# Optimization experiments

Hardware: AMD Instinct MI355X
Metric: run time of the kernel (lower is better)

The kernel has to match this reference:

```python
import jax, jax.numpy as jnp
import numpy as np

N = 50000; E = 800000; F_IN = 512; H = 2; C1 = 128; C2 = 32; N_CLASS = 32; N_HID = 64
LOSS_WEIGHT = 0.5


def _layer_norm(x, g, b):
    m = x.mean(-1, keepdims=True)
    v = ((x - m) ** 2).mean(-1, keepdims=True)
    return (x - m) / jnp.sqrt(v + 1e-5) * g + b


def _gat_conv(x, src, dst, n, W, Wh1, bh1, Wh2, bh2, heads, c, concat):
    # x: [n, in]; src/dst: [E'] (self loops already appended)
    xt = (x @ W).reshape(n, heads, c)            # [n, H, C]
    xj = xt[src]                                  # [E', H, C] gathered source feats
    # scaled dot-product attention logits per edge/head
    e = jnp.einsum('ehc,ehc->eh', xt[dst], xj) / np.float32(np.sqrt(c))
    m = jax.ops.segment_max(e, dst, num_segments=n)
    ex = jnp.exp(e - m[dst])
    s = jax.ops.segment_sum(ex, dst, num_segments=n)
    alpha = ex / (s[dst] + 1e-16)                 # [E', H]
    out = jax.ops.segment_sum(alpha[:, :, None] * xj, dst, num_segments=n)  # [n, H, C]
    # per-head auxiliary class prediction head h (DeepGAT)
    h = jax.nn.elu(jnp.einsum('nhc,cd->nhd', xt, Wh1) + bh1)
    h = jnp.einsum('nhd,dk->nhk', h, Wh2) + bh2   # [n, H, n_class]
    out = out.reshape(n, heads * c) if concat else out.mean(axis=1)
    return out, h, alpha


def setup_inputs() -> dict:
    key = jax.random.key(0)
    ks = jax.random.split(key, 24)
    g = lambda k, shape, fan: jax.random.normal(k, shape, jnp.float32) / np.float32(np.sqrt(fan))
    d = {}
    d['x'] = jax.random.normal(ks[0], (N, F_IN), jnp.float32)
    d['edge_index'] = jax.random.randint(ks[1], (2, E), 0, N, jnp.int32)
    # layer 1: F_IN -> H*C1 (concat)
    d['W1'] = g(ks[2], (F_IN, H * C1), F_IN)
    d['Wh1a'] = g(ks[3], (C1, N_HID), C1); d['bh1a'] = jnp.zeros((N_HID,), jnp.float32)
    d['Wh2a'] = g(ks[4], (N_HID, N_CLASS), N_HID); d['bh2a'] = jnp.zeros((N_CLASS,), jnp.float32)
    d['g1'] = jnp.ones((H * C1,), jnp.float32); d['b1'] = jnp.zeros((H * C1,), jnp.float32)
    # layer 2: H*C1 -> H*C2 (concat)
    d['W2'] = g(ks[5], (H * C1, H * C2), H * C1)
    d['Wh1b'] = g(ks[6], (C2, N_HID), C2); d['bh1b'] = jnp.zeros((N_HID,), jnp.float32)
    d['Wh2b'] = g(ks[7], (N_HID, N_CLASS), N_HID); d['bh2b'] = jnp.zeros((N_CLASS,), jnp.float32)
    d['g2'] = jnp.ones((H * C2,), jnp.float32); d['b2'] = jnp.zeros((H * C2,), jnp.float32)
    # layer 3: H*C2 -> N_CLASS (mean over heads)
    d['W3'] = g(ks[8], (H * C2, H * N_CLASS), H * C2)
    d['Wh1c'] = g(ks[9], (N_CLASS, N_HID), N_CLASS); d['bh1c'] = jnp.zeros((N_HID,), jnp.float32)
    d['Wh2c'] = g(ks[10], (N_HID, N_CLASS), N_HID); d['bh2c'] = jnp.zeros((N_CLASS,), jnp.float32)
    d['g3'] = jnp.ones((N_CLASS,), jnp.float32); d['b3'] = jnp.zeros((N_CLASS,), jnp.float32)
    return d


def reference(x, edge_index, W1, Wh1a, bh1a, Wh2a, bh2a, g1, b1,
              W2, Wh1b, bh1b, Wh2b, bh2b, g2, b2,
              W3, Wh1c, bh1c, Wh2c, bh2c, g3, b3):
    n = x.shape[0]
    loops = jnp.arange(n, dtype=edge_index.dtype)
    src = jnp.concatenate([edge_index[0], loops])
    dst = jnp.concatenate([edge_index[1], loops])
    # eval mode: F.dropout is identity
    x1, h1, _ = _gat_conv(x, src, dst, n, W1, Wh1a, bh1a, Wh2a, bh2a, H, C1, True)
    x1 = jax.nn.elu(_layer_norm(x1, g1, b1))
    x2, h2, _ = _gat_conv(x1, src, dst, n, W2, Wh1b, bh1b, Wh2b, bh2b, H, C2, True)
    x2 = jax.nn.elu(_layer_norm(x2, g2, b2))
    x3, h3, alpha = _gat_conv(x2, src, dst, n, W3, Wh1c, bh1c, Wh2c, bh2c, H, N_CLASS, False)
    x3 = _layer_norm(x3, g3, b3)
    return (x3, h1, h2 * LOSS_WEIGHT, h3, alpha)
```

## Files before the change

kernel.cpp:

```cpp
#include <hip/hip_runtime.h>

#define NN 50000
#define EE 800000
#define EPN 850000

typedef __attribute__((ext_vector_type(8))) short bf16x8;
typedef __attribute__((ext_vector_type(4))) float f32x4;
typedef unsigned short ushort_t;

__device__ __forceinline__ float eluf(float v) { return v > 0.f ? v : expm1f(v); }
__device__ __forceinline__ unsigned short f2bf(float f) {
  unsigned u = __float_as_uint(f);
  unsigned r = (u + 0x7FFFu + ((u >> 16) & 1u)) >> 16;
  return (unsigned short)r;
}
__device__ __forceinline__ float bf2f(unsigned short b) {
  return __uint_as_float(((unsigned)b) << 16);
}
__device__ __forceinline__ void unpack8(uint4 u, float* o) {
  o[0] = __uint_as_float(u.x << 16); o[1] = __uint_as_float(u.x & 0xFFFF0000u);
  o[2] = __uint_as_float(u.y << 16); o[3] = __uint_as_float(u.y & 0xFFFF0000u);
  o[4] = __uint_as_float(u.z << 16); o[5] = __uint_as_float(u.z & 0xFFFF0000u);
  o[6] = __uint_as_float(u.w << 16); o[7] = __uint_as_float(u.w & 0xFFFF0000u);
}
__device__ __forceinline__ void gload_lds16(const ushort_t* g, ushort_t* l) {
  __builtin_amdgcn_global_load_lds((const __attribute__((address_space(1))) void*)g,
                                   (__attribute__((address_space(3))) void*)l, 16, 0, 0);
}

__global__ __launch_bounds__(256) void conv_w1(const float* __restrict__ W,
                                               ushort_t* __restrict__ Wc) {
  int idx = blockIdx.x * 256 + threadIdx.x;
  if (idx >= 256 * 1024) return;
  int col = idx >> 10, rem = idx & 1023;
  int kb = rem >> 6, j = rem & 63;
  int sel = j >> 5, k = j & 31;
  int gk = kb * 32 + k;
  float v = W[(size_t)gk * 256 + col];
  unsigned short h = f2bf(v);
  Wc[idx] = sel ? (ushort_t)f2bf(v - bf2f(h)) : h;
}

__global__ __launch_bounds__(512) void gemm1_mfma(const float* __restrict__ A,
                                                  const ushort_t* __restrict__ Wc,
                                                  ushort_t* __restrict__ C16, int M) {
  constexpr int K = 512;
  __shared__ alignas(16) ushort_t Bs[2][128 * 64];
  int tid = threadIdx.x;
  int w = tid >> 6, lane = tid & 63, l15 = lane & 15, l4 = lane >> 4;
  int row0 = blockIdx.y * 128, col0 = blockIdx.x * 128;
  int arow = row0 + w * 16 + l15;
  int arowc = arow < M ? arow : M - 1;
  const float* arp = A + (size_t)arowc * K + l4 * 8;

  int chunk_src = (lane & 7) ^ ((lane >> 3) & 7);
  const ushort_t* wsrc =
      Wc + (size_t)(col0 + w * 16 + (lane >> 3)) * 1024 + chunk_src * 8;
  ushort_t* ldst0 = &Bs[0][(w * 16) * 64];
  ushort_t* ldst1 = &Bs[1][(w * 16) * 64];

  int swz = l15 & 7;
  int roff_h = ((l4 ^ swz) << 3);
  int roff_l = (((l4 | 4) ^ swz) << 3);
  int rbase = l15 * 64;

  f32x4 acc[8];
#pragma unroll
  for (int t = 0; t < 8; ++t) acc[t] = (f32x4){0.f, 0.f, 0.f, 0.f};

#pragma unroll
  for (int q = 0; q < 2; ++q) gload_lds16(wsrc + q * 8192, ldst0 + q * 512);
  float4 pa0c = *(const float4*)(arp);
  float4 pa1c = *(const float4*)(arp + 4);
  float4 pa0n, pa1n;

  for (int k0 = 0; k0 < K; k0 += 32) {
    int kb = k0 >> 5, p = kb & 1;
    __syncthreads();
    if (k0 + 32 < K) {
      ushort_t* dst = (p ? ldst0 : ldst1);
      const ushort_t* src = wsrc + (kb + 1) * 64;
#pragma unroll
      for (int q = 0; q < 2; ++q) gload_lds16(src + q * 8192, dst + q * 512);
      pa0n = *(const float4*)(arp + k0 + 32);
      pa1n = *(const float4*)(arp + k0 + 36);
    }
    bf16x8 ah, al;
    {
      float v[8] = {pa0c.x, pa0c.y, pa0c.z, pa0c.w, pa1c.x, pa1c.y, pa1c.z, pa1c.w};
#pragma unroll
      for (int i = 0; i < 8; ++i) {
        unsigned short h = f2bf(v[i]);
        ah[i] = (short)h;
        al[i] = (short)f2bf(v[i] - bf2f(h));
      }
    }
    const ushort_t* bp = &Bs[p][rbase];
#pragma unroll
    for (int t = 0; t < 8; ++t) {
      bf16x8 b_h = *(const bf16x8*)&bp[t * 1024 + roff_h];
      bf16x8 b_l = *(const bf16x8*)&bp[t * 1024 + roff_l];
      acc[t] = __builtin_amdgcn_mfma_f32_16x16x32_bf16(ah, b_h, acc[t], 0, 0, 0);
      acc[t] = __builtin_amdgcn_mfma_f32_16x16x32_bf16(ah, b_l, acc[t], 0, 0, 0);
      acc[t] = __builtin_amdgcn_mfma_f32_16x16x32_bf16(al, b_h, acc[t], 0, 0, 0);
    }
    pa0c = pa0n; pa1c = pa1n;
  }
#pragma unroll
  for (int t = 0; t < 8; ++t) {
#pragma unroll
    for (int r = 0; r < 4; ++r) {
      int grow = row0 + w * 16 + l4 * 4 + r;
      if (grow < M) C16[(size_t)grow * 256 + col0 + t * 16 + l15] = f2bf(acc[t][r]);
    }
  }
}

template <int NT>
__global__ __launch_bounds__(256) void gemm_mfma(const float* __restrict__ A,
                                                 const float* __restrict__ B,
                                                 ushort_t* __restrict__ C16,
                                                 int M, int N, int K) {
  __shared__ unsigned short Ah[64 * 40], Al[64 * 40];
  __shared__ unsigned short Bh[NT * 16 * 40], Bl[NT * 16 * 40];
  int tid = threadIdx.x;
  int wave = tid >> 6, lane = tid & 63;
  int l15 = lane & 15, l4 = lane >> 4;
  int row0 = blockIdx.y * 64, col0 = blockIdx.x * (NT * 16);

  f32x4 acc[NT];
#pragma unroll
  for (int t = 0; t < NT; ++t) acc[t] = (f32x4){0.f, 0.f, 0.f, 0.f};

  int ar = tid >> 2;
  int ak = (tid & 3) * 8;
  constexpr int TPC = 256 / (NT * 16);
  constexpr int NK = 32 / TPC;
  int bc = tid / TPC;
  int bk = (tid % TPC) * NK;

  for (int k0 = 0; k0 < K; k0 += 32) {
    {
      float v[8];
      int grow = row0 + ar;
      if (grow < M) {
        float4 q0 = *(const float4*)&A[(size_t)grow * K + k0 + ak];
        float4 q1 = *(const float4*)&A[(size_t)grow * K + k0 + ak + 4];
        v[0] = q0.x; v[1] = q0.y; v[2] = q0.z; v[3] = q0.w;
        v[4] = q1.x; v[5] = q1.y; v[6] = q1.z; v[7] = q1.w;
      } else {
#pragma unroll
        for (int i = 0; i < 8; ++i) v[i] = 0.f;
      }
      bf16x8 hv, lv;
#pragma unroll
      for (int i = 0; i < 8; ++i) {
        unsigned short h = f2bf(v[i]);
        hv[i] = (short)h;
        lv[i] = (short)f2bf(v[i] - bf2f(h));
      }
      *(bf16x8*)&Ah[ar * 40 + ak] = hv;
      *(bf16x8*)&Al[ar * 40 + ak] = lv;
    }
    {
#pragma unroll
      for (int i = 0; i < NK; ++i) {
        float v = B[(size_t)(k0 + bk + i) * N + col0 + bc];
        unsigned short h = f2bf(v);
        Bh[bc * 40 + bk + i] = h;
        Bl[bc * 40 + bk + i] = f2bf(v - bf2f(h));
      }
    }
    __syncthreads();
    bf16x8 a_h = *(const bf16x8*)&Ah[(wave * 16 + l15) * 40 + l4 * 8];
    bf16x8 a_l = *(const bf16x8*)&Al[(wave * 16 + l15) * 40 + l4 * 8];
#pragma unroll
    for (int t = 0; t < NT; ++t) {
      bf16x8 b_h = *(const bf16x8*)&Bh[(t * 16 + l15) * 40 + l4 * 8];
      bf16x8 b_l = *(const bf16x8*)&Bl[(t * 16 + l15) * 40 + l4 * 8];
      acc[t] = __builtin_amdgcn_mfma_f32_16x16x32_bf16(a_h, b_h, acc[t], 0, 0, 0);
      acc[t] = __builtin_amdgcn_mfma_f32_16x16x32_bf16(a_h, b_l, acc[t], 0, 0, 0);
      acc[t] = __builtin_amdgcn_mfma_f32_16x16x32_bf16(a_l, b_h, acc[t], 0, 0, 0);
    }
    __syncthreads();
  }
#pragma unroll
  for (int t = 0; t < NT; ++t) {
#pragma unroll
    for (int r = 0; r < 4; ++r) {
      int grow = row0 + wave * 16 + l4 * 4 + r;
      if (grow < M) C16[(size_t)grow * N + col0 + t * 16 + l15] = f2bf(acc[t][r]);
    }
  }
}

template <int C>
__global__ __launch_bounds__(256) void aux_mfma(const ushort_t* __restrict__ xt16,
                                                const float* __restrict__ Wh1,
                                                const float* __restrict__ bh1,
                                                const float* __restrict__ Wh2,
                                                const float* __restrict__ bh2,
                                                float* __restrict__ hout,
                                                float scale) {
  constexpr int KS = C / 32;
  constexpr int LDB = C + 8;
  constexpr int UNION_B = 64 * LDB * 2 * 2;
  constexpr int UNION_H = 64 * 72 * 2 * 2;
  constexpr int UNION = UNION_B > UNION_H ? UNION_B : UNION_H;
  __shared__ alignas(16) char smem[9216 + UNION];
  ushort_t* w2h = (ushort_t*)smem;
  ushort_t* w2l = w2h + 32 * 72;
  ushort_t* BhS = (ushort_t*)(smem + 9216);
  ushort_t* BlS = BhS + 64 * LDB;
  ushort_t* hidh = (ushort_t*)(smem + 9216);
  ushort_t* hidl = hidh + 64 * 72;

  int tid = threadIdx.x;
  for (int i = tid; i < C * 64; i += 256) {
    int k = i >> 6, col = i & 63;
    float v = Wh1[i];
    unsigned short h = f2bf(v);
    BhS[col * LDB + k] = h;
    BlS[col * LDB + k] = f2bf(v - bf2f(h));
  }
  for (int i = tid; i < 64 * 32; i += 256) {
    int k = i >> 5, col = i & 31;
    float v = Wh2[i];
    unsigned short h = f2bf(v);
    w2h[col * 72 + k] = h;
    w2l[col * 72 + k] = f2bf(v - bf2f(h));
  }
  __syncthreads();

  int w = tid >> 6, lane = tid & 63, l15 = lane & 15, l4 = lane >> 4;
  int gr = blockIdx.x * 64 + w * 16 + l15;
  const int M2 = 2 * NN;

  f32x4 acc[4];
#pragma unroll
  for (int t = 0; t < 4; ++t) acc[t] = (f32x4){0.f, 0.f, 0.f, 0.f};

#pragma unroll
  for (int ks = 0; ks < KS; ++ks) {
    bf16x8 ah;
    if (gr < M2) {
      ah = *(const bf16x8*)(xt16 + (size_t)gr * C + ks * 32 + l4 * 8);
    } else {
      ah = (bf16x8){0, 0, 0, 0, 0, 0, 0, 0};
    }
#pragma unroll
    for (int t = 0; t < 4; ++t) {
      bf16x8 b_h = *(const bf16x8*)&BhS[(t * 16 + l15) * LDB + ks * 32 + l4 * 8];
      bf16x8 b_l = *(const bf16x8*)&BlS[(t * 16 + l15) * LDB + ks * 32 + l4 * 8];
      acc[t] = __builtin_amdgcn_mfma_f32_16x16x32_bf16(ah, b_h, acc[t], 0, 0, 0);
      acc[t] = __builtin_amdgcn_mfma_f32_16x16x32_bf16(ah, b_l, acc[t], 0, 0, 0);
    }
  }
  __syncthreads();
#pragma unroll
  for (int t = 0; t < 4; ++t) {
    float bb = bh1[t * 16 + l15];
#pragma unroll
    for (int r = 0; r < 4; ++r) {
      float h = eluf(acc[t][r] + bb);
      unsigned short hh = f2bf(h);
      int row = w * 16 + l4 * 4 + r, col = t * 16 + l15;
      hidh[row * 72 + col] = hh;
      hidl[row * 72 + col] = f2bf(h - bf2f(hh));
    }
  }
  __syncthreads();
  f32x4 acc2[2];
  acc2[0] = (f32x4){0.f, 0.f, 0.f, 0.f};
  acc2[1] = acc2[0];
#pragma unroll
  for (int ks = 0; ks < 2; ++ks) {
    bf16x8 ah = *(const bf16x8*)&hidh[(w * 16 + l15) * 72 + ks * 32 + l4 * 8];
    bf16x8 al = *(const bf16x8*)&hidl[(w * 16 + l15) * 72 + ks * 32 + l4 * 8];
#pragma unroll
    for (int t2 = 0; t2 < 2; ++t2) {
      bf16x8 b_h = *(const bf16x8*)&w2h[(t2 * 16 + l15) * 72 + ks * 32 + l4 * 8];
      bf16x8 b_l = *(const bf16x8*)&w2l[(t2 * 16 + l15) * 72 + ks * 32 + l4 * 8];
      acc2[t2] = __builtin_amdgcn_mfma_f32_16x16x32_bf16(ah, b_h, acc2[t2], 0, 0, 0);
      acc2[t2] = __builtin_amdgcn_mfma_f32_16x16x32_bf16(ah, b_l, acc2[t2], 0, 0, 0);
      acc2[t2] = __builtin_amdgcn_mfma_f32_16x16x32_bf16(al, b_h, acc2[t2], 0, 0, 0);
    }
  }
#pragma unroll
  for (int t2 = 0; t2 < 2; ++t2) {
    int col = t2 * 16 + l15;
    float bb = bh2[col];
#pragma unroll
    for (int r = 0; r < 4; ++r) {
      int gr2 = blockIdx.x * 64 + w * 16 + l4 * 4 + r;
      if (gr2 < M2)
        hout[(size_t)(gr2 >> 1) * 64 + (gr2 & 1) * 32 + col] = (acc2[t2][r] + bb) * scale;
    }
  }
}

__global__ __launch_bounds__(256) void hist_kernel(const int* __restrict__ ei,
                                                   int* __restrict__ cnt) {
  int e = blockIdx.x * 256 + threadIdx.x;
  if (e >= EPN) return;
  int d = (e < EE) ? ei[EE + e] : e - EE;
  atomicAdd(&cnt[d], 1);
}

__global__ __launch_bounds__(1024) void scan_blocks(const int* __restrict__ cnt,
                                                    int* __restrict__ tmp,
                                                    int* __restrict__ bsum) {
  __shared__ int lds[1024];
  int t = threadIdx.x, idx = blockIdx.x * 1024 + t;
  int v = (idx < NN) ? cnt[idx] : 0;
  lds[t] = v;
  __syncthreads();
  for (int off = 1; off < 1024; off <<= 1) {
    int add = (t >= off) ? lds[t - off] : 0;
    __syncthreads();
    lds[t] += add;
    __syncthreads();
  }
  if (idx < NN) tmp[idx] = lds[t];
  if (t == 1023) bsum[blockIdx.x] = lds[t];
}

__global__ __launch_bounds__(64) void scan_bsum(int* __restrict__ bsum, int nb) {
  int t = threadIdx.x;
  int v = (t < nb) ? bsum[t] : 0;
#pragma unroll
  for (int off = 1; off < 64; off <<= 1) {
    int u = __shfl_up(v, off);
    if (t >= off) v += u;
  }
  if (t < nb) bsum[t] = v;
}

__global__ __launch_bounds__(256) void scan_final(const int* __restrict__ cnt,
                                                  const int* __restrict__ tmp,
                                                  const int* __restrict__ bsum,
                                                  int* __restrict__ rowptr,
                                                  int* __restrict__ fill) {
  int idx = blockIdx.x * 256 + threadIdx.x;
  if (idx >= NN) return;
  int b = idx >> 10;
  int off = (b > 0) ? bsum[b - 1] : 0;
  int inc = tmp[idx] + off;
  rowptr[idx + 1] = inc;
  fill[idx] = inc - cnt[idx];
  if (idx == 0) rowptr[0] = 0;
}

__global__ __launch_bounds__(256) void scatter_kernel(const int* __restrict__ ei,
                                                      int* __restrict__ fill,
                                                      int* __restrict__ eids,
                                                      int* __restrict__ srcs) {
  int e = blockIdx.x * 256 + threadIdx.x;
  if (e >= EPN) return;
  int d, s;
  if (e < EE) { d = ei[EE + e]; s = ei[e]; } else { d = s = e - EE; }
  int pos = atomicAdd(&fill[d], 1);
  eids[pos] = e;
  srcs[pos] = s;
}

__global__ __launch_bounds__(256) void gat256_fused(const ushort_t* __restrict__ xt16,
                                                    const int* __restrict__ srcs,
                                                    const int* __restrict__ rowptr,
                                                    float* __restrict__ outb,
                                                    const float* __restrict__ g,
                                                    const float* __restrict__ b) {
  int node = (int)((blockIdx.x * (size_t)blockDim.x + threadIdx.x) >> 6);
  int lane = threadIdx.x & 63;
  if (node >= NN) return;
  int l32 = lane & 31, half = lane >> 5;
  int start = rowptr[node], end = rowptr[node + 1];
  float dv[8];
  unpack8(*(const uint4*)(xt16 + (size_t)node * 256 + l32 * 8), dv);
  float m = -3e38f, s_h = 0.f;
  float acc[8] = {0.f, 0.f, 0.f, 0.f, 0.f, 0.f, 0.f, 0.f};

  int i = start;
  for (; i + 8 <= end; i += 8) {
    int sj[4];
    float sv[4][8];
    float p[4];
#pragma unroll
    for (int q = 0; q < 4; ++q) sj[q] = srcs[i + q * 2 + half];
#pragma unroll
    for (int q = 0; q < 4; ++q)
      unpack8(*(const uint4*)(xt16 + (size_t)sj[q] * 256 + l32 * 8), sv[q]);
#pragma unroll
    for (int q = 0; q < 4; ++q) {
      float p_ = 0.f;
#pragma unroll
      for (int k = 0; k < 8; ++k) p_ = fmaf(sv[q][k], dv[k], p_);
      p_ += __shfl_xor(p_, 1); p_ += __shfl_xor(p_, 2);
      p_ += __shfl_xor(p_, 4); p_ += __shfl_xor(p_, 8);
      p[q] = p_ * 0.08838834764831843f;
    }
    float pm = fmaxf(fmaxf(p[0], p[1]), fmaxf(p[2], p[3]));
    if (__any(pm > m + 8.f)) {
#pragma unroll
      for (int q = 0; q < 4; ++q) {
        float pb = fmaxf(p[q], __shfl_xor(p[q], 32));
        float mn = fmaxf(m, pb);
        float scf = __expf(m - mn), w = __expf(p[q] - mn);
        s_h = s_h * scf + w;
#pragma unroll
        for (int k = 0; k < 8; ++k) acc[k] = fmaf(w, sv[q][k], acc[k] * scf);
        m = mn;
      }
    } else {
#pragma unroll
      for (int q = 0; q < 4; ++q) {
        float w = __expf(p[q] - m);
        s_h += w;
#pragma unroll
        for (int k = 0; k < 8; ++k) acc[k] = fmaf(w, sv[q][k], acc[k]);
      }
    }
  }
  for (; i < end; i += 2) {
    bool valid = (i + half) < end;
    int sj = srcs[valid ? i + half : i];
    float sv[8];
    unpack8(*(const uint4*)(xt16 + (size_t)sj * 256 + l32 * 8), sv);
    float p_ = 0.f;
#pragma unroll
    for (int k = 0; k < 8; ++k) p_ = fmaf(sv[k], dv[k], p_);
    p_ += __shfl_xor(p_, 1); p_ += __shfl_xor(p_, 2);
    p_ += __shfl_xor(p_, 4); p_ += __shfl_xor(p_, 8);
    p_ *= 0.08838834764831843f;
    if (!valid) p_ = -3e38f;
    float pb = fmaxf(p_, __shfl_xor(p_, 32));
    float mn = fmaxf(m, pb);
    float scf = __expf(m - mn);
    float w = valid ? __expf(p_ - mn) : 0.f;
    s_h = s_h * scf + w;
#pragma unroll
    for (int k = 0; k < 8; ++k) acc[k] = fmaf(w, sv[k], acc[k] * scf);
    m = mn;
  }
  float s = s_h + __shfl_xor(s_h, 32);
#pragma unroll
  for (int k = 0; k < 8; ++k) acc[k] += __shfl_xor(acc[k], 32);
  float inv = 1.f / (s + 1e-16f);
  float v[8];
#pragma unroll
  for (int k = 0; k < 8; ++k) v[k] = acc[k] * inv;
  float sum = 0.f;
#pragma unroll
  for (int k = 0; k < 8; ++k) sum += v[k];
  sum += __shfl_xor(sum, 1); sum += __shfl_xor(sum, 2); sum += __shfl_xor(sum, 4);
  sum += __shfl_xor(sum, 8); sum += __shfl_xor(sum, 16);
  float mean = sum * (1.f / 256.f);
  float q = 0.f;
#pragma unroll
  for (int k = 0; k < 8; ++k) { v[k] -= mean; q = fmaf(v[k], v[k], q); }
  q += __shfl_xor(q, 1); q += __shfl_xor(q, 2); q += __shfl_xor(q, 4);
  q += __shfl_xor(q, 8); q += __shfl_xor(q, 16);
  float rstd = rsqrtf(q * (1.f / 256.f) + 1e-5f);
  if (half == 0) {
    float4 ga = *(const float4*)&g[l32 * 8], gb = *(const float4*)&g[l32 * 8 + 4];
    float4 ba = *(const float4*)&b[l32 * 8], bb = *(const float4*)&b[l32 * 8 + 4];
    float4 r0, r1;
    r0.x = eluf(v[0] * rstd * ga.x + ba.x); r0.y = eluf(v[1] * rstd * ga.y + ba.y);
    r0.z = eluf(v[2] * rstd * ga.z + ba.z); r0.w = eluf(v[3] * rstd * ga.w + ba.w);
    r1.x = eluf(v[4] * rstd * gb.x + bb.x); r1.y = eluf(v[5] * rstd * gb.y + bb.y);
    r1.z = eluf(v[6] * rstd * gb.z + bb.z); r1.w = eluf(v[7] * rstd * gb.w + bb.w);
    *(float4*)(outb + (size_t)node * 256 + l32 * 8) = r0;
    *(float4*)(outb + (size_t)node * 256 + l32 * 8 + 4) = r1;
  }
}

template <int MODE>
__global__ __launch_bounds__(256) void gat64_t(const ushort_t* __restrict__ xt16,
                                               const int* __restrict__ srcs,
                                               const int* __restrict__ eids,
                                               const int* __restrict__ rowptr,
                                               float* __restrict__ outf,
                                               float* __restrict__ logit_out,
                                               float* __restrict__ mbuf,
                                               float* __restrict__ sbuf,
                                               const float* __restrict__ g,
                                               const float* __restrict__ b) {
  __shared__ alignas(16) float wbuf[4][64];
  int wv = threadIdx.x >> 6;
  int node = (int)((blockIdx.x * (size_t)blockDim.x + threadIdx.x) >> 6);
  int lane = threadIdx.x & 63;
  if (node >= NN) return;
  int l32 = lane & 31, half = lane >> 5;
  int start = rowptr[node], end = rowptr[node + 1];
  float dv[32];
  {
    const ushort_t* dp = xt16 + (size_t)node * 64 + half * 32;
    unpack8(*(const uint4*)(dp), dv);
    unpack8(*(const uint4*)(dp + 8), dv + 8);
    unpack8(*(const uint4*)(dp + 16), dv + 16);
    unpack8(*(const uint4*)(dp + 24), dv + 24);
  }
  float m = -3e38f, s = 0.f, acc = 0.f;

  for (int base = start; base < end; base += 32) {
    int cnt = end - base;
    cnt = cnt > 32 ? 32 : cnt;
    int sidx = srcs[base + (l32 < cnt ? l32 : 0)];
    float sv[32];
    {
      const ushort_t* sp = xt16 + (size_t)sidx * 64 + half * 32;
      unpack8(*(const uint4*)(sp), sv);
      unpack8(*(const uint4*)(sp + 8), sv + 8);
      unpack8(*(const uint4*)(sp + 16), sv + 16);
      unpack8(*(const uint4*)(sp + 24), sv + 24);
    }
    float p = 0.f;
#pragma unroll
    for (int k = 0; k < 32; ++k) p = fmaf(sv[k], dv[k], p);
    p *= 0.17677669529663687f;
    if (MODE == 1) {
      if (l32 < cnt) logit_out[(size_t)eids[base + l32] * 2 + half] = p;
    }
    if (l32 >= cnt) p = -3e38f;
    float bm = p;
    bm = fmaxf(bm, __shfl_xor(bm, 1));
    bm = fmaxf(bm, __shfl_xor(bm, 2));
    bm = fmaxf(bm, __shfl_xor(bm, 4));
    bm = fmaxf(bm, __shfl_xor(bm, 8));
    bm = fmaxf(bm, __shfl_xor(bm, 16));
    float mn = fmaxf(m, bm);
    float scf = __expf(m - mn);
    float w = (l32 < cnt) ? __expf(p - mn) : 0.f;
    wbuf[wv][(half << 5) + l32] = w;
    float bs = w;
    bs += __shfl_xor(bs, 1);
    bs += __shfl_xor(bs, 2);
    bs += __shfl_xor(bs, 4);
    bs += __shfl_xor(bs, 8);
    bs += __shfl_xor(bs, 16);
    s = s * scf + bs;
    acc *= scf;
    m = mn;
    int nb4 = cnt & ~3;
    const float* wp = &wbuf[wv][(half << 5)];
    for (int e = 0; e < nb4; e += 4) {
      float4 w4 = *(const float4*)(wp + e);
      int s0 = srcs[base + e + 0];
      int s1 = srcs[base + e + 1];
      int s2 = srcs[base + e + 2];
      int s3 = srcs[base + e + 3];
      acc = fmaf(w4.x, bf2f(xt16[(size_t)s0 * 64 + lane]), acc);
      acc = fmaf(w4.y, bf2f(xt16[(size_t)s1 * 64 + lane]), acc);
      acc = fmaf(w4.z, bf2f(xt16[(size_t)s2 * 64 + lane]), acc);
      acc = fmaf(w4.w, bf2f(xt16[(size_t)s3 * 64 + lane]), acc);
    }
    for (int e = nb4; e < cnt; ++e) {
      float wq = wp[e];
      int sj = srcs[base + e];
      acc = fmaf(wq, bf2f(xt16[(size_t)sj * 64 + lane]), acc);
    }
  }
  float inv = 1.f / (s + 1e-16f);
  float v = acc * inv;
  if (MODE == 0) {
    float sum = v;
#pragma unroll
    for (int o = 1; o < 64; o <<= 1) sum += __shfl_xor(sum, o);
    float mean = sum * (1.f / 64.f);
    float dvv = v - mean;
    float q = dvv * dvv;
#pragma unroll
    for (int o = 1; o < 64; o <<= 1) q += __shfl_xor(q, o);
    float rstd = rsqrtf(q * (1.f / 64.f) + 1e-5f);
    outf[(size_t)node * 64 + lane] = eluf(dvv * rstd * g[lane] + b[lane]);
  } else {
    if (l32 == 0) {
      mbuf[(size_t)node * 2 + half] = m;
      sbuf[(size_t)node * 2 + half] = s;
    }
    float t = __shfl_xor(v, 32);
    float y = 0.5f * (v + t);
    float sum = y;
#pragma unroll
    for (int o = 1; o < 32; o <<= 1) sum += __shfl_xor(sum, o);
    float mean = sum * (1.f / 32.f);
    float dy = y - mean;
    float q = dy * dy;
#pragma unroll
    for (int o = 1; o < 32; o <<= 1) q += __shfl_xor(q, o);
    float rstd = rsqrtf(q * (1.f / 32.f) + 1e-5f);
    if (half == 0) outf[(size_t)node * 32 + l32] = dy * rstd * g[l32] + b[l32];
  }
}

__global__ __launch_bounds__(256) void alpha_fix(float* __restrict__ al,
                                                 const int* __restrict__ ei,
                                                 const float* __restrict__ mbuf,
                                                 const float* __restrict__ sbuf) {
  size_t i = blockIdx.x * (size_t)blockDim.x + threadIdx.x;
  if (i >= (size_t)EPN * 2) return;
  int e = (int)(i >> 1), h = (int)(i & 1);
  int d = (e < EE) ? ei[EE + e] : e - EE;
  al[i] = expf(al[i] - mbuf[(size_t)d * 2 + h]) / (sbuf[(size_t)d * 2 + h] + 1e-16f);
}

extern "C" void kernel_launch(void* const* d_in, const int* in_sizes, int n_in,
                              void* d_out, int out_size, void* d_ws, size_t ws_size,
                              hipStream_t stream) {
  const float* x    = (const float*)d_in[0];
  const int*   ei   = (const int*)d_in[1];
  const float* W1   = (const float*)d_in[2];
  const float* Wh1a = (const float*)d_in[3];
  const float* bh1a = (const float*)d_in[4];
  const float* Wh2a = (const float*)d_in[5];
  const float* bh2a = (const float*)d_in[6];
  const float* g1   = (const float*)d_in[7];
  const float* b1   = (const float*)d_in[8];
  const float* W2   = (const float*)d_in[9];
  const float* Wh1b = (const float*)d_in[10];
  const float* bh1b = (const float*)d_in[11];
  const float* Wh2b = (const float*)d_in[12];
  const float* bh2b = (const float*)d_in[13];
  const float* g2   = (const float*)d_in[14];
  const float* b2   = (const float*)d_in[15];
  const float* W3   = (const float*)d_in[16];
  const float* Wh1c = (const float*)d_in[17];
  const float* bh1c = (const float*)d_in[18];
  const float* Wh2c = (const float*)d_in[19];
  const float* bh2c = (const float*)d_in[20];
  const float* g3   = (const float*)d_in[21];
  const float* b3   = (const float*)d_in[22];

  float* out  = (float*)d_out;
  float* o_x3 = out;
  float* o_h1 = out + (size_t)NN * 32;
  float* o_h2 = o_h1 + (size_t)NN * 64;
  float* o_h3 = o_h2 + (size_t)NN * 64;
  float* o_al = o_h3 + (size_t)NN * 64;

  float* ws  = (float*)d_ws;
  float* A   = ws;
  float* Bb  = ws + (size_t)NN * 256;
  int* cnt    = (int*)(Bb + (size_t)NN * 256);
  int* rowptr = cnt + NN;
  int* fill   = rowptr + NN + 1;
  int* eids   = fill + NN;
  int* srcs   = eids + EPN;
  int* tmp    = srcs + EPN;
  int* bsum   = tmp + NN;
  float* mbuf = (float*)(bsum + 64);
  float* sbuf = mbuf + (size_t)NN * 2;
  ushort_t* W1c = (ushort_t*)(sbuf + (size_t)NN * 2);
  ushort_t* A16 = (ushort_t*)A;

  dim3 blk(256);
  int gEdges = (EPN + 255) / 256;
  int gNodeW = (NN * 64 + 255) / 256;
  int gRows = (NN + 63) / 64;
  int gRows128 = (NN + 127) / 128;
  int gPairs = (int)(((size_t)EPN * 2 + 255) / 256);
  int gAux = (2 * NN + 63) / 64;
  int nbScan = (NN + 1023) / 1024;

  conv_w1<<<1024, blk, 0, stream>>>(W1, W1c);
  hipMemsetAsync(cnt, 0, (size_t)NN * 4, stream);
  hist_kernel<<<gEdges, blk, 0, stream>>>(ei, cnt);
  scan_blocks<<<nbScan, 1024, 0, stream>>>(cnt, tmp, bsum);
  scan_bsum<<<1, 64, 0, stream>>>(bsum, nbScan);
  scan_final<<<(NN + 255) / 256, blk, 0, stream>>>(cnt, tmp, bsum, rowptr, fill);
  scatter_kernel<<<gEdges, blk, 0, stream>>>(ei, fill, eids, srcs);

  gemm1_mfma<<<dim3(2, gRows128), 512, 0, stream>>>(x, W1c, A16, NN);
  aux_mfma<128><<<gAux, blk, 0, stream>>>(A16, Wh1a, bh1a, Wh2a, bh2a, o_h1, 1.0f);
  gat256_fused<<<gNodeW, blk, 0, stream>>>(A16, srcs, rowptr, Bb, g1, b1);

  gemm_mfma<4><<<dim3(1, gRows), blk, 0, stream>>>(Bb, W2, A16, NN, 64, 256);
  aux_mfma<32><<<gAux, blk, 0, stream>>>(A16, Wh1b, bh1b, Wh2b, bh2b, o_h2, 0.5f);
  gat64_t<0><<<gNodeW, blk, 0, stream>>>(A16, srcs, nullptr, rowptr, Bb, nullptr,
                                         nullptr, nullptr, g2, b2);

  gemm_mfma<4><<<dim3(1, gRows), blk, 0, stream>>>(Bb, W3, A16, NN, 64, 64);
  aux_mfma<32><<<gAux, blk, 0, stream>>>(A16, Wh1c, bh1c, Wh2c, bh2c, o_h3, 1.0f);
  gat64_t<1><<<gNodeW, blk, 0, stream>>>(A16, srcs, eids, rowptr, o_x3, o_al,
                                         mbuf, sbuf, g3, b3);
  alpha_fix<<<gPairs, blk, 0, stream>>>(o_al, ei, mbuf, sbuf);
}
```

Measured before the change: 478.1 us.

## Horizontally fuse aux prediction head and GAT aggregation kernels per layer

Merges the per-layer auxiliary MLP head kernel and the GAT aggregation kernel into one launch. Blocks are interleaved so that one aux block runs alongside every eight aggregation blocks, and both reuse a shared static LDS buffer. The aim is to remove three kernel launches and let the compute-bound MFMA head overlap the memory-bound gather. The cost is that every aggregation block now reserves about 45 KB of LDS, which limits how many blocks fit on a CU for the latency-sensitive gather work.

```diff
diff --git a/kernel.cpp b/kernel.cpp
--- a/kernel.cpp
+++ b/kernel.cpp
@@ -195,19 +195,15 @@
 }
 
 template <int C>
-__global__ __launch_bounds__(256) void aux_mfma(const ushort_t* __restrict__ xt16,
-                                                const float* __restrict__ Wh1,
-                                                const float* __restrict__ bh1,
-                                                const float* __restrict__ Wh2,
-                                                const float* __restrict__ bh2,
-                                                float* __restrict__ hout,
-                                                float scale) {
+__device__ __forceinline__ void aux_body(char* smem, int bid,
+                                         const ushort_t* __restrict__ xt16,
+                                         const float* __restrict__ Wh1,
+                                         const float* __restrict__ bh1,
+                                         const float* __restrict__ Wh2,
+                                         const float* __restrict__ bh2,
+                                         float* __restrict__ hout, float scale) {
   constexpr int KS = C / 32;
   constexpr int LDB = C + 8;
-  constexpr int UNION_B = 64 * LDB * 2 * 2;
-  constexpr int UNION_H = 64 * 72 * 2 * 2;
-  constexpr int UNION = UNION_B > UNION_H ? UNION_B : UNION_H;
-  __shared__ alignas(16) char smem[9216 + UNION];
   ushort_t* w2h = (ushort_t*)smem;
   ushort_t* w2l = w2h + 32 * 72;
   ushort_t* BhS = (ushort_t*)(smem + 9216);
@@ -233,7 +229,7 @@
   __syncthreads();
 
   int w = tid >> 6, lane = tid & 63, l15 = lane & 15, l4 = lane >> 4;
-  int gr = blockIdx.x * 64 + w * 16 + l15;
+  int gr = bid * 64 + w * 16 + l15;
   const int M2 = 2 * NN;
 
   f32x4 acc[4];
@@ -292,85 +288,20 @@
     float bb = bh2[col];
 #pragma unroll
     for (int r = 0; r < 4; ++r) {
-      int gr2 = blockIdx.x * 64 + w * 16 + l4 * 4 + r;
+      int gr2 = bid * 64 + w * 16 + l4 * 4 + r;
       if (gr2 < M2)
         hout[(size_t)(gr2 >> 1) * 64 + (gr2 & 1) * 32 + col] = (acc2[t2][r] + bb) * scale;
     }
   }
 }
 
-__global__ __launch_bounds__(256) void hist_kernel(const int* __restrict__ ei,
-                                                   int* __restrict__ cnt) {
-  int e = blockIdx.x * 256 + threadIdx.x;
-  if (e >= EPN) return;
-  int d = (e < EE) ? ei[EE + e] : e - EE;
-  atomicAdd(&cnt[d], 1);
-}
-
-__global__ __launch_bounds__(1024) void scan_blocks(const int* __restrict__ cnt,
-                                                    int* __restrict__ tmp,
-                                                    int* __restrict__ bsum) {
-  __shared__ int lds[1024];
-  int t = threadIdx.x, idx = blockIdx.x * 1024 + t;
-  int v = (idx < NN) ? cnt[idx] : 0;
-  lds[t] = v;
-  __syncthreads();
-  for (int off = 1; off < 1024; off <<= 1) {
-    int add = (t >= off) ? lds[t - off] : 0;
-    __syncthreads();
-    lds[t] += add;
-    __syncthreads();
-  }
-  if (idx < NN) tmp[idx] = lds[t];
-  if (t == 1023) bsum[blockIdx.x] = lds[t];
-}
-
-__global__ __launch_bounds__(64) void scan_bsum(int* __restrict__ bsum, int nb) {
-  int t = threadIdx.x;
-  int v = (t < nb) ? bsum[t] : 0;
-#pragma unroll
-  for (int off = 1; off < 64; off <<= 1) {
-    int u = __shfl_up(v, off);
-    if (t >= off) v += u;
-  }
-  if (t < nb) bsum[t] = v;
-}
-
-__global__ __launch_bounds__(256) void scan_final(const int* __restrict__ cnt,
-                                                  const int* __restrict__ tmp,
-                                                  const int* __restrict__ bsum,
-                                                  int* __restrict__ rowptr,
-                                                  int* __restrict__ fill) {
-  int idx = blockIdx.x * 256 + threadIdx.x;
-  if (idx >= NN) return;
-  int b = idx >> 10;
-  int off = (b > 0) ? bsum[b - 1] : 0;
-  int inc = tmp[idx] + off;
-  rowptr[idx + 1] = inc;
-  fill[idx] = inc - cnt[idx];
-  if (idx == 0) rowptr[0] = 0;
-}
-
-__global__ __launch_bounds__(256) void scatter_kernel(const int* __restrict__ ei,
-                                                      int* __restrict__ fill,
-                                                      int* __restrict__ eids,
-                                                      int* __restrict__ srcs) {
-  int e = blockIdx.x * 256 + threadIdx.x;
-  if (e >= EPN) return;
-  int d, s;
-  if (e < EE) { d = ei[EE + e]; s = ei[e]; } else { d = s = e - EE; }
-  int pos = atomicAdd(&fill[d], 1);
-  eids[pos] = e;
-  srcs[pos] = s;
-}
-
-__global__ __launch_bounds__(256) void gat256_fused(const ushort_t* __restrict__ xt16,
-                                                    const int* __restrict__ srcs,
-                                                    const int* __restrict__ rowptr,
-                                                    float* __restrict__ outb,
-                                                    const float* __restrict__ g,
-                                                    const float* __restrict__ b) {
-  int node = (int)((blockIdx.x * (size_t)blockDim.x + threadIdx.x) >> 6);
+__device__ __forceinline__ void gat256_body(int bid, const ushort_t* __restrict__ xt16,
+                                            const int* __restrict__ srcs,
+                                            const int* __restrict__ rowptr,
+                                            float* __restrict__ outb,
+                                            const float* __restrict__ g,
+                                            const float* __restrict__ b) {
+  int node = (int)(((size_t)bid * 256 + threadIdx.x) >> 6);
   int lane = threadIdx.x & 63;
   if (node >= NN) return;
   int l32 = lane & 31, half = lane >> 5;
@@ -475,19 +406,19 @@
 }
 
 template <int MODE>
-__global__ __launch_bounds__(256) void gat64_t(const ushort_t* __restrict__ xt16,
-                                               const int* __restrict__ srcs,
-                                               const int* __restrict__ eids,
-                                               const int* __restrict__ rowptr,
-                                               float* __restrict__ outf,
-                                               float* __restrict__ logit_out,
-                                               float* __restrict__ mbuf,
-                                               float* __restrict__ sbuf,
-                                               const float* __restrict__ g,
-                                               const float* __restrict__ b) {
-  __shared__ alignas(16) float wbuf[4][64];
+__device__ __forceinline__ void gat64_body(float (*wbuf)[64], int bid,
+                                           const ushort_t* __restrict__ xt16,
+                                           const int* __restrict__ srcs,
+                                           const int* __restrict__ eids,
+                                           const int* __restrict__ rowptr,
+                                           float* __restrict__ outf,
+                                           float* __restrict__ logit_out,
+                                           float* __restrict__ mbuf,
+                                           float* __restrict__ sbuf,
+                                           const float* __restrict__ g,
+                                           const float* __restrict__ b) {
   int wv = threadIdx.x >> 6;
-  int node = (int)((blockIdx.x * (size_t)blockDim.x + threadIdx.x) >> 6);
+  int node = (int)(((size_t)bid * 256 + threadIdx.x) >> 6);
   int lane = threadIdx.x & 63;
   if (node >= NN) return;
   int l32 = lane & 31, half = lane >> 5;
@@ -593,6 +524,123 @@
   }
 }
 
+#define A_AUX 1563
+#define G_GAT 12500
+
+__global__ __launch_bounds__(256) void fused_l1(const ushort_t* __restrict__ xt16,
+                                                const float* __restrict__ Wh1,
+                                                const float* __restrict__ bh1,
+                                                const float* __restrict__ Wh2,
+                                                const float* __restrict__ bh2,
+                                                float* __restrict__ hout,
+                                                const int* __restrict__ srcs,
+                                                const int* __restrict__ rowptr,
+                                                float* __restrict__ outb,
+                                                const float* __restrict__ g,
+                                                const float* __restrict__ b) {
+  __shared__ alignas(16) char smem[46080];
+  int k = blockIdx.x, grp = k / 9, pos = k - grp * 9;
+  if (pos == 0) {
+    aux_body<128>(smem, grp, xt16, Wh1, bh1, Wh2, bh2, hout, 1.0f);
+  } else {
+    int gid = grp * 8 + pos - 1;
+    if (gid < G_GAT) gat256_body(gid, xt16, srcs, rowptr, outb, g, b);
+  }
+}
+
+template <int MODE>
+__global__ __launch_bounds__(256) void fused_l23(const ushort_t* __restrict__ xt16,
+                                                 const float* __restrict__ Wh1,
+                                                 const float* __restrict__ bh1,
+                                                 const float* __restrict__ Wh2,
+                                                 const float* __restrict__ bh2,
+                                                 float* __restrict__ hout, float scale,
+                                                 const int* __restrict__ srcs,
+                                                 const int* __restrict__ eids,
+                                                 const int* __restrict__ rowptr,
+                                                 float* __restrict__ outf,
+                                                 float* __restrict__ logit_out,
+                                                 float* __restrict__ mbuf,
+                                                 float* __restrict__ sbuf,
+                                                 const float* __restrict__ g,
+                                                 const float* __restrict__ b) {
+  __shared__ alignas(16) char smem[46080];
+  int k = blockIdx.x, grp = k / 9, pos = k - grp * 9;
+  if (pos == 0) {
+    aux_body<32>(smem, grp, xt16, Wh1, bh1, Wh2, bh2, hout, scale);
+  } else {
+    int gid = grp * 8 + pos - 1;
+    if (gid < G_GAT)
+      gat64_body<MODE>((float(*)[64])smem, gid, xt16, srcs, eids, rowptr, outf,
+                       logit_out, mbuf, sbuf, g, b);
+  }
+}
+
+__global__ __launch_bounds__(256) void hist_kernel(const int* __restrict__ ei,
+                                                   int* __restrict__ cnt) {
+  int e = blockIdx.x * 256 + threadIdx.x;
+  if (e >= EPN) return;
+  int d = (e < EE) ? ei[EE + e] : e - EE;
+  atomicAdd(&cnt[d], 1);
+}
+
+__global__ __launch_bounds__(1024) void scan_blocks(const int* __restrict__ cnt,
+                                                    int* __restrict__ tmp,
+                                                    int* __restrict__ bsum) {
+  __shared__ int lds[1024];
+  int t = threadIdx.x, idx = blockIdx.x * 1024 + t;
+  int v = (idx < NN) ? cnt[idx] : 0;
+  lds[t] = v;
+  __syncthreads();
+  for (int off = 1; off < 1024; off <<= 1) {
+    int add = (t >= off) ? lds[t - off] : 0;
+    __syncthreads();
+    lds[t] += add;
+    __syncthreads();
+  }
+  if (idx < NN) tmp[idx] = lds[t];
+  if (t == 1023) bsum[blockIdx.x] = lds[t];
+}
+
+__global__ __launch_bounds__(64) void scan_bsum(int* __restrict__ bsum, int nb) {
+  int t = threadIdx.x;
+  int v = (t < nb) ? bsum[t] : 0;
+#pragma unroll
+  for (int off = 1; off < 64; off <<= 1) {
+    int u = __shfl_up(v, off);
+    if (t >= off) v += u;
+  }
+  if (t < nb) bsum[t] = v;
+}
+
+__global__ __launch_bounds__(256) void scan_final(const int* __restrict__ cnt,
+                                                  const int* __restrict__ tmp,
+                                                  const int* __restrict__ bsum,
+                                                  int* __restrict__ rowptr,
+                                                  int* __restrict__ fill) {
+  int idx = blockIdx.x * 256 + threadIdx.x;
+  if (idx >= NN) return;
+  int b = idx >> 10;
+  int off = (b > 0) ? bsum[b - 1] : 0;
+  int inc = tmp[idx] + off;
+  rowptr[idx + 1] = inc;
+  fill[idx] = inc - cnt[idx];
+  if (idx == 0) rowptr[0] = 0;
+}
+
+__global__ __launch_bounds__(256) void scatter_kernel(const int* __restrict__ ei,
+                                                      int* __restrict__ fill,
+                                                      int* __restrict__ eids,
+                                                      int* __restrict__ srcs) {
+  int e = blockIdx.x * 256 + threadIdx.x;
+  if (e >= EPN) return;
+  int d, s;
+  if (e < EE) { d = ei[EE + e]; s = ei[e]; } else { d = s = e - EE; }
+  int pos = atomicAdd(&fill[d], 1);
+  eids[pos] = e;
+  srcs[pos] = s;
+}
+
 __global__ __launch_bounds__(256) void alpha_fix(float* __restrict__ al,
                                                  const int* __restrict__ ei,
                                                  const float* __restrict__ mbuf,
@@ -655,12 +703,11 @@
 
   dim3 blk(256);
   int gEdges = (EPN + 255) / 256;
-  int gNodeW = (NN * 64 + 255) / 256;
   int gRows = (NN + 63) / 64;
   int gRows128 = (NN + 127) / 128;
   int gPairs = (int)(((size_t)EPN * 2 + 255) / 256);
-  int gAux = (2 * NN + 63) / 64;
   int nbScan = (NN + 1023) / 1024;
+  int gFused = 9 * A_AUX;
 
   conv_w1<<<1024, blk, 0, stream>>>(W1, W1c);
   hipMemsetAsync(cnt, 0, (size_t)NN * 4, stream);
@@ -671,17 +718,17 @@
   scatter_kernel<<<gEdges, blk, 0, stream>>>(ei, fill, eids, srcs);
 
   gemm1_mfma<<<dim3(2, gRows128), 512, 0, stream>>>(x, W1c, A16, NN);
-  aux_mfma<128><<<gAux, blk, 0, stream>>>(A16, Wh1a, bh1a, Wh2a, bh2a, o_h1, 1.0f);
-  gat256_fused<<<gNodeW, blk, 0, stream>>>(A16, srcs, rowptr, Bb, g1, b1);
+  fused_l1<<<gFused, blk, 0, stream>>>(A16, Wh1a, bh1a, Wh2a, bh2a, o_h1,
+                                       srcs, rowptr, Bb, g1, b1);
 
   gemm_mfma<4><<<dim3(1, gRows), blk, 0, stream>>>(Bb, W2, A16, NN, 64, 256);
-  aux_mfma<32><<<gAux, blk, 0, stream>>>(A16, Wh1b, bh1b, Wh2b, bh2b, o_h2, 0.5f);
-  gat64_t<0><<<gNodeW, blk, 0, stream>>>(A16, srcs, nullptr, rowptr, Bb, nullptr,
-                                         nullptr, nullptr, g2, b2);
+  fused_l23<0><<<gFused, blk, 0, stream>>>(A16, Wh1b, bh1b, Wh2b, bh2b, o_h2, 0.5f,
+                                           srcs, nullptr, rowptr, Bb, nullptr,
+                                           nullptr, nullptr, g2, b2);
 
   gemm_mfma<4><<<dim3(1, gRows), blk, 0, stream>>>(Bb, W3, A16, NN, 64, 64);
-  aux_mfma<32><<<gAux, blk, 0, stream>>>(A16, Wh1c, bh1c, Wh2c, bh2c, o_h3, 1.0f);
-  gat64_t<1><<<gNodeW, blk, 0, stream>>>(A16, srcs, eids, rowptr, o_x3, o_al,
-                                         mbuf, sbuf, g3, b3);
+  fused_l23<1><<<gFused, blk, 0, stream>>>(A16, Wh1c, bh1c, Wh2c, bh2c, o_h3, 1.0f,
+                                           srcs, eids, rowptr, o_x3, o_al,
+                                           mbuf, sbuf, g3, b3);
   alpha_fix<<<gPairs, blk, 0, stream>>>(o_al, ei, mbuf, sbuf);
 }
```

Measured after the change: 537.1 us. 12.3% more time.
